# Performance work log

Measured on AMD Instinct MI355X. Metric: run time of the kernel, lower is better.

The kernel has to match this reference:

```python
import jax, jax.numpy as jnp
import numpy as np
import math

B, Q, CQ = 2, 2048, 512
H, D = 8, 64  # no_heads, c_hidden

def setup_inputs() -> dict:
    key = jax.random.key(0)
    ks = jax.random.split(key, 8)
    s = 0.02
    return {
        "q_x": jax.random.normal(ks[0], (B, Q, CQ), jnp.float32),
        "kv_x": jax.random.normal(ks[1], (B, Q, CQ), jnp.float32),
        "bias": jax.random.normal(ks[2], (B, 1, Q, Q), jnp.float32),
        "w_qkv": jax.random.normal(ks[3], (3 * H * D, CQ), jnp.float32) * s,
        "w_o": jax.random.normal(ks[4], (CQ, H * D), jnp.float32) * s,
        "b_o": jnp.zeros((CQ,), jnp.float32),
        "w_g": jax.random.normal(ks[5], (H * D, CQ), jnp.float32) * s,
        "b_g": jnp.zeros((H * D,), jnp.float32),
    }

def reference(q_x, kv_x, bias, w_qkv, w_o, b_o, w_g, b_g):
    # Fused QKV projection from q_x (kv_x is unused by the original module's _prep_qkv)
    qkv = jnp.einsum('bqc,ec->bqe', q_x, w_qkv)  # [B,Q,3*H*D]
    q, k, v = jnp.split(qkv, 3, axis=-1)
    q = q.reshape(B, Q, H, D) / math.sqrt(D)
    k = k.reshape(B, Q, H, D)
    v = v.reshape(B, Q, H, D)
    # scores + additive pairwise bias, softmax over keys
    scores = jnp.einsum('bqhd,bkhd->bhqk', q, k) + bias  # [B,H,Q,K]
    attn = jax.nn.softmax(scores, axis=-1)
    o = jnp.einsum('bhqk,bkhd->bqhd', attn, v)  # [B,Q,H,D]
    # sigmoid gating
    g = jax.nn.sigmoid(jnp.einsum('bqc,ec->bqe', q_x, w_g) + b_g).reshape(B, Q, H, D)
    o = o * g
    # output projection
    o = o.reshape(B, Q, H * D)
    return jnp.einsum('bqe,ce->bqc', o, w_o) + b_o
```

## Files before the change

### kernel.cpp

```cpp
#include <hip/hip_runtime.h>
#include <math.h>

#define B_  2
#define Q_  2048
#define CQ_ 512
#define H_  8
#define D_  64
#define M_  (B_*Q_)
#define L2E 1.44269504088896f

typedef __bf16 bf16;
typedef __bf16 bf16x4 __attribute__((ext_vector_type(4)));
typedef __bf16 bf16x8 __attribute__((ext_vector_type(8)));
typedef float  f32x4  __attribute__((ext_vector_type(4)));
typedef float  f32x16 __attribute__((ext_vector_type(16)));
typedef unsigned int u32x2 __attribute__((ext_vector_type(2)));

__device__ __forceinline__ void gl_lds16(const bf16* g, bf16* l) {
    __builtin_amdgcn_global_load_lds(
        (const __attribute__((address_space(1))) unsigned int*)g,
        (__attribute__((address_space(3))) unsigned int*)l, 16, 0, 0);
}

__device__ __forceinline__ unsigned int cvtpk_bf16(float lo, float hi) {
    unsigned int r;
    asm("v_cvt_pk_bf16_f32 %0, %1, %2" : "=v"(r) : "v"(lo), "v"(hi));
    return r;
}

#define S0 (4096*512)
#define S1 (1536*512)
#define S2 (512*512)
#define S3 (512*512)
#define NCV ((S0 + S1 + S2 + S3) / (256 * 8))
__global__ __launch_bounds__(256)
void convert_kernel(const float* __restrict__ qx, const float* __restrict__ wqkv,
                    const float* __restrict__ wg, const float* __restrict__ wo,
                    const float* __restrict__ bias,
                    bf16* __restrict__ qxb, bf16* __restrict__ wcat,
                    bf16* __restrict__ wob, float* __restrict__ bT)
{
    __shared__ float lds[2048];
    const int bx = blockIdx.x;
    const int t  = threadIdx.x;
    if (bx < NCV) {
        const long long e = ((long long)bx * 256 + t) * 8;
        const float* src; bf16* dst;
        if (e < S0)                { src = qx + e;                  dst = qxb + e; }
        else if (e < S0 + S1)      { src = wqkv + (e - S0);         dst = wcat + (e - S0); }
        else if (e < S0 + S1 + S2) { src = wg + (e - S0 - S1);      dst = wcat + S1 + (e - S0 - S1); }
        else                       { src = wo + (e - S0 - S1 - S2); dst = wob + (e - S0 - S1 - S2); }
        const float4 a = *(const float4*)(src);
        const float4 b = *(const float4*)(src + 4);
        bf16x8 v;
        v[0] = (bf16)a.x; v[1] = (bf16)a.y; v[2] = (bf16)a.z; v[3] = (bf16)a.w;
        v[4] = (bf16)b.x; v[5] = (bf16)b.y; v[6] = (bf16)b.z; v[7] = (bf16)b.w;
        *(bf16x8*)dst = v;
    } else {
        const int x = bx - NCV;
        const int b = x >> 11, q32 = (x >> 5) & 63, kt = x & 31;
        const int qo = t >> 3, kc = (t & 7) * 8;
        const float* src = bias + ((size_t)b * Q_ + q32 * 32 + qo) * Q_ + kt * 64 + kc;
        const float4 a = *(const float4*)src;
        const float4 c = *(const float4*)(src + 4);
        const float v[8] = {a.x, a.y, a.z, a.w, c.x, c.y, c.z, c.w};
        #pragma unroll
        for (int j2 = 0; j2 < 8; ++j2) {
            const int ko = kc + j2;
            const int i  = (ko >> 5) * 4 + ((ko >> 3) & 3);
            const int b5 = (ko >> 2) & 1;
            const int j  = ko & 3;
            lds[i * 256 + b5 * 128 + qo * 4 + j] = v[j2] * L2E;
        }
        __syncthreads();
        float* outp = bT + ((size_t)(b * 64 + q32) * 32 + kt) * 2048 + t * 8;
        *(float4*)(outp)     = *(const float4*)(lds + t * 8);
        *(float4*)(outp + 4) = *(const float4*)(lds + t * 8 + 4);
    }
}

template<int BM, int BN>
__global__ __launch_bounds__(256)
void gemm_bf16(const bf16* __restrict__ A, const bf16* __restrict__ W,
               const float* __restrict__ bvec,
               bf16* __restrict__ qb, bf16* __restrict__ kb, bf16* __restrict__ vb,
               bf16* __restrict__ gb)
{
    constexpr int MI = BM / 32, NJ = BN / 32;
    __shared__ __align__(16) bf16 As[BM * 32];
    __shared__ __align__(16) bf16 Bs[BN * 32];

    const int t = threadIdx.x;
    const int w = t >> 6, lane = t & 63;
    const int l15 = lane & 15, quad = lane >> 4;
    const int wm = w & 1, wn = w >> 1;
    const int bm = blockIdx.x * BM;
    const int bn = blockIdx.y * BN;
    const bool swapped = ((bn >> 9) != 2);

    f32x4 acc[MI][NJ] = {};

    const int rr = t >> 2;
    const int cc = (t & 3) * 8;

    for (int k0 = 0; k0 < 512; k0 += 32) {
        #pragma unroll
        for (int i = 0; i < BM / 64; ++i)
            gl_lds16(A + (size_t)(bm + i * 64 + rr) * 512 + k0 + cc,
                     As + (i * 64 + w * 16) * 32);
        #pragma unroll
        for (int i = 0; i < BN / 64; ++i)
            gl_lds16(W + (size_t)(bn + i * 64 + rr) * 512 + k0 + cc,
                     Bs + (i * 64 + w * 16) * 32);
        __asm__ volatile("s_waitcnt vmcnt(0)" ::: "memory");
        __syncthreads();

        bf16x8 af[MI], bfr[NJ];
        #pragma unroll
        for (int i = 0; i < MI; ++i)
            af[i] = *(const bf16x8*)(As + (wm * (BM / 2) + i * 16 + l15) * 32 + quad * 8);
        #pragma unroll
        for (int j = 0; j < NJ; ++j)
            bfr[j] = *(const bf16x8*)(Bs + (wn * (BN / 2) + j * 16 + l15) * 32 + quad * 8);
        if (swapped) {
            #pragma unroll
            for (int i = 0; i < MI; ++i)
                #pragma unroll
                for (int j = 0; j < NJ; ++j)
                    acc[i][j] = __builtin_amdgcn_mfma_f32_16x16x32_bf16(bfr[j], af[i], acc[i][j], 0, 0, 0);
        } else {
            #pragma unroll
            for (int i = 0; i < MI; ++i)
                #pragma unroll
                for (int j = 0; j < NJ; ++j)
                    acc[i][j] = __builtin_amdgcn_mfma_f32_16x16x32_bf16(af[i], bfr[j], acc[i][j], 0, 0, 0);
        }
        __syncthreads();
    }

    if (swapped) {
        #pragma unroll
        for (int i = 0; i < MI; ++i) {
            const int m = bm + wm * (BM / 2) + i * 16 + l15;
            const int b = m >> 11, qq = m & 2047;
            #pragma unroll
            for (int j = 0; j < NJ; ++j) {
                const int n0 = bn + wn * (BN / 2) + j * 16 + quad * 4;
                const f32x4 cv = acc[i][j];
                const int part = n0 >> 9;
                if (part == 0) {
                    const int h = (n0 >> 6) & 7, d0 = n0 & 63;
                    bf16x4 q4;
                    #pragma unroll
                    for (int r = 0; r < 4; ++r) q4[r] = (bf16)(cv[r] * (0.125f * L2E));
                    *(bf16x4*)(qb + (size_t)(b * H_ + h) * (Q_ * D_) + (size_t)qq * 64 + d0) = q4;
                } else if (part == 1) {
                    const int h = (n0 >> 6) & 7, d0 = n0 & 63;
                    const size_t off = (size_t)(b * H_ + h) * (Q_ * D_)
                        + (qq >> 6) * 4096 + ((qq >> 5) & 1) * 2048
                        + (d0 >> 4) * 512 + ((d0 >> 3) & 1) * 256
                        + (qq & 31) * 8 + (d0 & 7);
                    bf16x4 k4;
                    #pragma unroll
                    for (int r = 0; r < 4; ++r) k4[r] = (bf16)cv[r];
                    *(bf16x4*)(kb + off) = k4;
                } else {
                    const int gcol = n0 & 511;
                    const float4 bv4 = *(const float4*)(bvec + gcol);
                    bf16x4 g4;
                    g4[0] = (bf16)(1.f / (1.f + __expf(-(cv[0] + bv4.x))));
                    g4[1] = (bf16)(1.f / (1.f + __expf(-(cv[1] + bv4.y))));
                    g4[2] = (bf16)(1.f / (1.f + __expf(-(cv[2] + bv4.z))));
                    g4[3] = (bf16)(1.f / (1.f + __expf(-(cv[3] + bv4.w))));
                    *(bf16x4*)(gb + (size_t)m * 512 + gcol) = g4;
                }
            }
        }
    } else {
        #pragma unroll
        for (int i = 0; i < MI; ++i) {
            const int m0 = bm + wm * (BM / 2) + i * 16 + quad * 4;
            const int b = m0 >> 11, qq0 = m0 & 2047;
            #pragma unroll
            for (int j = 0; j < NJ; ++j) {
                const int n = bn + wn * (BN / 2) + j * 16 + l15;
                const int h = (n >> 6) & 7, d = n & 63;
                const size_t off = (size_t)(b * H_ + h) * (Q_ * D_)
                    + (qq0 >> 6) * 4096 + (d >> 5) * 2048
                    + ((qq0 & 63) >> 4) * 512 + ((qq0 >> 3) & 1) * 256
                    + (d & 31) * 8 + (qq0 & 7);
                bf16x4 v4;
                #pragma unroll
                for (int r = 0; r < 4; ++r) v4[r] = (bf16)acc[i][j][r];
                *(bf16x4*)(vb + off) = v4;
            }
        }
    }
}

__global__ __launch_bounds__(256, 3)
void attn_part(const bf16* __restrict__ qb, const bf16* __restrict__ kf,
               const bf16* __restrict__ vf, const float* __restrict__ bT,
               bf16* __restrict__ po, float2* __restrict__ ml)
{
    __shared__ __align__(16) bf16 Ks[2][4096];
    __shared__ __align__(16) bf16 Vs[2][4096];

    const int tid  = threadIdx.x;
    const int wv   = tid >> 6, lane = tid & 63;
    const int l31  = lane & 31, b5 = lane >> 5;
    const int x    = blockIdx.x;
    const int bh   = ((x & 7) << 1) | (x >> 3);
    const int b    = bh >> 3;
    const int qg   = blockIdx.y * 128 + wv * 32 + l31;
    const int ks   = blockIdx.z;
    const int t0   = ks * 11;
    const int nt   = (ks < 2) ? 11 : 10;

    const bf16* qp = qb + ((size_t)bh * Q_ + qg) * D_;
    bf16x8 bq[4];
    #pragma unroll
    for (int c = 0; c < 4; ++c)
        bq[c] = *(const bf16x8*)(qp + c * 16 + b5 * 8);

    f32x16 acc[2] = {};
    float m_run = -INFINITY, l_run = 0.f;

    const bf16*  kfb  = kf + (size_t)bh * (Q_ * D_) + (size_t)t0 * 4096;
    const bf16*  vfb  = vf + (size_t)bh * (Q_ * D_) + (size_t)t0 * 4096;
    const int q32 = blockIdx.y * 4 + wv;
    const float* brow = bT + (((size_t)b * 64 + q32) * 32 + t0) * 2048;

    f32x4 nb[8];

    #pragma unroll
    for (int p = 0; p < 2; ++p) {
        gl_lds16(kfb + (wv * 2 + p) * 512 + lane * 8, Ks[0] + (wv * 2 + p) * 512);
        gl_lds16(vfb + (wv * 2 + p) * 512 + lane * 8, Vs[0] + (wv * 2 + p) * 512);
    }
    #pragma unroll
    for (int i = 0; i < 8; ++i)
        nb[i] = *(const f32x4*)(brow + i * 256 + lane * 4);
    __asm__ volatile("s_waitcnt vmcnt(0)" ::: "memory");
    __syncthreads();

    int cur = 0;
    #pragma unroll 1
    for (int t = 0; t < nt; ++t) {
        if (t < nt - 1) {
            const size_t off = (size_t)(t + 1) * 4096;
            #pragma unroll
            for (int p = 0; p < 2; ++p) {
                gl_lds16(kfb + off + (wv * 2 + p) * 512 + lane * 8,
                         Ks[cur ^ 1] + (wv * 2 + p) * 512);
                gl_lds16(vfb + off + (wv * 2 + p) * 512 + lane * 8,
                         Vs[cur ^ 1] + (wv * 2 + p) * 512);
            }
        }
        __asm__ volatile("" ::: "memory");

        f32x16 sv[2];
        #pragma unroll
        for (int kg = 0; kg < 2; ++kg)
            #pragma unroll
            for (int r = 0; r < 16; ++r)
                sv[kg][r] = nb[kg * 4 + (r >> 2)][r & 3];

        if (t < nt - 1) {
            const float* bnx = brow + (size_t)(t + 1) * 2048;
            #pragma unroll
            for (int i = 0; i < 8; ++i)
                nb[i] = *(const f32x4*)(bnx + i * 256 + lane * 4);
        }
        __asm__ volatile("" ::: "memory");

        const bf16* Kc = Ks[cur];
        __builtin_amdgcn_s_setprio(1);
        #pragma unroll
        for (int kg = 0; kg < 2; ++kg)
            #pragma unroll
            for (int c = 0; c < 4; ++c) {
                const bf16x8 ak = *(const bf16x8*)(Kc + kg * 2048 + c * 512 + lane * 8);
                sv[kg] = __builtin_amdgcn_mfma_f32_32x32x16_bf16(ak, bq[c], sv[kg], 0, 0, 0);
            }
        __builtin_amdgcn_s_setprio(0);

        float mx[16];
        #pragma unroll
        for (int r = 0; r < 16; ++r) mx[r] = fmaxf(sv[0][r], sv[1][r]);
        #pragma unroll
        for (int r = 0; r < 8; ++r) mx[r] = fmaxf(mx[r], mx[r + 8]);
        #pragma unroll
        for (int r = 0; r < 4; ++r) mx[r] = fmaxf(mx[r], mx[r + 4]);
        float tmax = fmaxf(fmaxf(mx[0], mx[1]), fmaxf(mx[2], mx[3]));
        tmax = fmaxf(tmax, __shfl_xor(tmax, 32, 64));

        const float m_old = m_run;
        const bool keep = (__all(tmax <= m_old + 8.f) != 0);
        const float mn = keep ? m_old : fmaxf(m_old, tmax);
        m_run = mn;

        #pragma unroll
        for (int kg = 0; kg < 2; ++kg)
            #pragma unroll
            for (int r = 0; r < 16; ++r)
                sv[kg][r] = __builtin_amdgcn_exp2f(sv[kg][r] - mn);

        float sm[16];
        #pragma unroll
        for (int r = 0; r < 16; ++r) sm[r] = sv[0][r] + sv[1][r];
        #pragma unroll
        for (int r = 0; r < 8; ++r) sm[r] += sm[r + 8];
        #pragma unroll
        for (int r = 0; r < 4; ++r) sm[r] += sm[r + 4];
        float rsum = (sm[0] + sm[1]) + (sm[2] + sm[3]);
        rsum += __shfl_xor(rsum, 32, 64);
        if (keep) {
            l_run += rsum;
        } else {
            const float alpha = __builtin_amdgcn_exp2f(m_old - mn);
            l_run = l_run * alpha + rsum;
            acc[0] *= alpha;
            acc[1] *= alpha;
        }

        bf16x8 bp[4];
        #pragma unroll
        for (int kg = 0; kg < 2; ++kg)
            #pragma unroll
            for (int h = 0; h < 2; ++h) {
                const unsigned int u  = cvtpk_bf16(sv[kg][8 * h + 0], sv[kg][8 * h + 1]);
                const unsigned int u2 = cvtpk_bf16(sv[kg][8 * h + 2], sv[kg][8 * h + 3]);
                const unsigned int vv = cvtpk_bf16(sv[kg][8 * h + 4], sv[kg][8 * h + 5]);
                const unsigned int v2 = cvtpk_bf16(sv[kg][8 * h + 6], sv[kg][8 * h + 7]);
                const u32x2 s1 = __builtin_amdgcn_permlane32_swap(u,  vv, false, false);
                const u32x2 s2 = __builtin_amdgcn_permlane32_swap(u2, v2, false, false);
                union { unsigned int w[4]; bf16x8 v8; } pkw;
                pkw.w[0] = s1[0]; pkw.w[1] = s2[0]; pkw.w[2] = s1[1]; pkw.w[3] = s2[1];
                bp[kg * 2 + h] = pkw.v8;
            }

        const bf16* Vc = Vs[cur];
        __builtin_amdgcn_s_setprio(1);
        #pragma unroll
        for (int c4 = 0; c4 < 4; ++c4) {
            #pragma unroll
            for (int dg = 0; dg < 2; ++dg) {
                const bf16x8 av = *(const bf16x8*)(Vc + dg * 2048 + c4 * 512 + lane * 8);
                acc[dg] = __builtin_amdgcn_mfma_f32_32x32x16_bf16(av, bp[c4], acc[dg], 0, 0, 0);
            }
        }
        __builtin_amdgcn_s_setprio(0);

        __asm__ volatile("s_waitcnt vmcnt(8)" ::: "memory");
        __syncthreads();
        cur ^= 1;
    }

    const float inv = 1.f / l_run;
    const size_t pbase = ((size_t)(ks * 16 + bh) * Q_ + qg) * 64;
    #pragma unroll
    for (int dg = 0; dg < 2; ++dg)
        #pragma unroll
        for (int gi = 0; gi < 4; ++gi) {
            const int d0 = dg * 32 + gi * 8 + b5 * 4;
            bf16x4 ov;
            #pragma unroll
            for (int r = 0; r < 4; ++r)
                ov[r] = (bf16)(acc[dg][gi * 4 + r] * inv);
            *(bf16x4*)(po + pbase + d0) = ov;
        }
    if (b5 == 0)
        ml[(size_t)(ks * 16 + bh) * Q_ + qg] = make_float2(m_run, l_run);
}

__global__ __launch_bounds__(256)
void gemm_out(const bf16* __restrict__ po, const float2* __restrict__ ml,
              const bf16* __restrict__ gb, const bf16* __restrict__ W,
              const float* __restrict__ bvec, float* __restrict__ fout)
{
    constexpr int BM = 64, BN = 128, MI = BM / 32, NJ = BN / 32;
    __shared__ __align__(16) bf16 As[BM * 32];
    __shared__ __align__(16) bf16 Bs[BN * 32];

    const int t = threadIdx.x;
    const int w = t >> 6, lane = t & 63;
    const int l15 = lane & 15, quad = lane >> 4;
    const int wm = w & 1, wn = w >> 1;
    const int bm = blockIdx.x * BM;
    const int bn = blockIdx.y * BN;

    const int rr = t >> 2;
    const int cc = (t & 3) * 8;
    const int m  = bm + rr;
    const int b  = m >> 11, qq = m & 2047;

    f32x4 acc[MI][NJ] = {};

    for (int k0 = 0; k0 < 512; k0 += 32) {
        #pragma unroll
        for (int i = 0; i < BN / 64; ++i)
            gl_lds16(W + (size_t)(bn + i * 64 + rr) * 512 + k0 + cc,
                     Bs + (i * 64 + w * 16) * 32);

        {
            const int c0 = k0 + cc;
            const int h  = c0 >> 6, d8 = c0 & 63;
            const int prow = (b * 8 + h) * 2048 + qq;
            const float2 m0 = ml[prow];
            const float2 m1 = ml[32768 + prow];
            const float2 m2 = ml[65536 + prow];
            const float Mx = fmaxf(fmaxf(m0.x, m1.x), m2.x);
            float w0 = m0.y * __builtin_amdgcn_exp2f(m0.x - Mx);
            float w1 = m1.y * __builtin_amdgcn_exp2f(m1.x - Mx);
            float w2 = m2.y * __builtin_amdgcn_exp2f(m2.x - Mx);
            const float inv = 1.f / (w0 + w1 + w2);
            w0 *= inv; w1 *= inv; w2 *= inv;
            const bf16x8 p0 = *(const bf16x8*)(po + (size_t)prow * 64 + d8);
            const bf16x8 p1 = *(const bf16x8*)(po + (size_t)(32768 + prow) * 64 + d8);
            const bf16x8 p2 = *(const bf16x8*)(po + (size_t)(65536 + prow) * 64 + d8);
            const bf16x8 gv = *(const bf16x8*)(gb + (size_t)m * 512 + c0);
            bf16x8 av;
            #pragma unroll
            for (int r = 0; r < 8; ++r)
                av[r] = (bf16)(((float)p0[r] * w0 + (float)p1[r] * w1 +
                                (float)p2[r] * w2) * (float)gv[r]);
            *(bf16x8*)(As + t * 8) = av;
        }

        __asm__ volatile("s_waitcnt vmcnt(0)" ::: "memory");
        __syncthreads();

        bf16x8 af[MI], bfr[NJ];
        #pragma unroll
        for (int i = 0; i < MI; ++i)
            af[i] = *(const bf16x8*)(As + (wm * (BM / 2) + i * 16 + l15) * 32 + quad * 8);
        #pragma unroll
        for (int j = 0; j < NJ; ++j)
            bfr[j] = *(const bf16x8*)(Bs + (wn * (BN / 2) + j * 16 + l15) * 32 + quad * 8);
        #pragma unroll
        for (int i = 0; i < MI; ++i)
            #pragma unroll
            for (int j = 0; j < NJ; ++j)
                acc[i][j] = __builtin_amdgcn_mfma_f32_16x16x32_bf16(bfr[j], af[i], acc[i][j], 0, 0, 0);
        __syncthreads();
    }

    #pragma unroll
    for (int i = 0; i < MI; ++i) {
        const int mm = bm + wm * (BM / 2) + i * 16 + l15;
        #pragma unroll
        for (int j = 0; j < NJ; ++j) {
            const int n0 = bn + wn * (BN / 2) + j * 16 + quad * 4;
            const f32x4 cv = acc[i][j];
            float4 st;
            st.x = cv[0] + bvec[n0 + 0];
            st.y = cv[1] + bvec[n0 + 1];
            st.z = cv[2] + bvec[n0 + 2];
            st.w = cv[3] + bvec[n0 + 3];
            *(float4*)(fout + (size_t)mm * 512 + n0) = st;
        }
    }
}

extern "C" void kernel_launch(void* const* d_in, const int* in_sizes, int n_in,
                              void* d_out, int out_size, void* d_ws, size_t ws_size,
                              hipStream_t stream)
{
    const float* q_x   = (const float*)d_in[0];
    const float* bias  = (const float*)d_in[2];
    const float* w_qkv = (const float*)d_in[3];
    const float* w_o   = (const float*)d_in[4];
    const float* b_o   = (const float*)d_in[5];
    const float* w_g   = (const float*)d_in[6];
    const float* b_g   = (const float*)d_in[7];
    float* out = (float*)d_out;

    char* ws = (char*)d_ws;
    bf16*   qxb  = (bf16*)(ws);
    bf16*   wcat = (bf16*)(ws + (4u  << 20));
    bf16*   po   = (bf16*)(ws);
    bf16*   qb   = (bf16*)(ws + (16u << 20));
    bf16*   kb   = (bf16*)(ws + (20u << 20));
    bf16*   vb   = (bf16*)(ws + (24u << 20));
    bf16*   gb   = (bf16*)(ws + (28u << 20));
    bf16*   wob  = (bf16*)(ws + (36u << 20));
    float2* ml   = (float2*)(ws + (36u << 20) + (1u << 19));
    float*  bT   = (float*)(ws + (38u << 20));

    convert_kernel<<<NCV + B_ * 64 * 32, 256, 0, stream>>>(
        q_x, w_qkv, w_g, w_o, bias, qxb, wcat, wob, bT);
    gemm_bf16<128, 128><<<dim3(32, 16), 256, 0, stream>>>(
        qxb, wcat, b_g, qb, kb, vb, gb);
    attn_part<<<dim3(B_ * H_, Q_ / 128, 3), 256, 0, stream>>>(qb, kb, vb, bT, po, ml);
    gemm_out<<<dim3(64, 4), 256, 0, stream>>>(po, ml, gb, wob, b_o, out);
}
```

Before: 178.4 us.

## Ping-pong bias prefetch registers in attention, software-prefetch gated A operands in output GEMM

The attention loop is unrolled by two and alternates between two bias register sets, so the next tile's bias prefetch no longer needs a register copy. The row-max reduction is regrouped into three-input max chains, and the block barrier becomes explicit waitcnt plus s_barrier with scheduling fences. In the output projection GEMM, the partial outputs, softmax stats and gate loads for the next K-step are issued before the barrier. A partial vmcnt wait lets those loads overlap the MFMA work instead of stalling on vmcnt(0) every iteration. This raises register pressure, and the final prefetch reads slightly past the last iteration's data, possibly past the end of the gate buffer for the last row.

```diff
diff --git a/kernel.cpp b/kernel.cpp
--- a/kernel.cpp
+++ b/kernel.cpp
@@ -231,7 +231,7 @@
     const int q32 = blockIdx.y * 4 + wv;
     const float* brow = bT + (((size_t)b * 64 + q32) * 32 + t0) * 2048;
 
-    f32x4 nb[8];
+    f32x4 nbA[8], nbB[8];
 
     #pragma unroll
     for (int p = 0; p < 2; ++p) {
@@ -240,13 +240,12 @@
     }
     #pragma unroll
     for (int i = 0; i < 8; ++i)
-        nb[i] = *(const f32x4*)(brow + i * 256 + lane * 4);
+        nbA[i] = *(const f32x4*)(brow + i * 256 + lane * 4);
     __asm__ volatile("s_waitcnt vmcnt(0)" ::: "memory");
     __syncthreads();
 
-    int cur = 0;
-    #pragma unroll 1
-    for (int t = 0; t < nt; ++t) {
+    auto step = [&](int t, f32x4 (&nbc)[8], f32x4 (&nbn)[8]) {
+        const int cur = t & 1;
         if (t < nt - 1) {
             const size_t off = (size_t)(t + 1) * 4096;
             #pragma unroll
@@ -264,13 +263,13 @@
         for (int kg = 0; kg < 2; ++kg)
             #pragma unroll
             for (int r = 0; r < 16; ++r)
-                sv[kg][r] = nb[kg * 4 + (r >> 2)][r & 3];
+                sv[kg][r] = nbc[kg * 4 + (r >> 2)][r & 3];
 
         if (t < nt - 1) {
             const float* bnx = brow + (size_t)(t + 1) * 2048;
             #pragma unroll
             for (int i = 0; i < 8; ++i)
-                nb[i] = *(const f32x4*)(bnx + i * 256 + lane * 4);
+                nbn[i] = *(const f32x4*)(bnx + i * 256 + lane * 4);
         }
         __asm__ volatile("" ::: "memory");
 
@@ -285,14 +284,17 @@
             }
         __builtin_amdgcn_s_setprio(0);
 
-        float mx[16];
-        #pragma unroll
-        for (int r = 0; r < 16; ++r) mx[r] = fmaxf(sv[0][r], sv[1][r]);
-        #pragma unroll
-        for (int r = 0; r < 8; ++r) mx[r] = fmaxf(mx[r], mx[r + 8]);
-        #pragma unroll
-        for (int r = 0; r < 4; ++r) mx[r] = fmaxf(mx[r], mx[r + 4]);
-        float tmax = fmaxf(fmaxf(mx[0], mx[1]), fmaxf(mx[2], mx[3]));
+        float a[8];
+        #pragma unroll
+        for (int r = 0; r < 8; ++r)
+            a[r] = fmaxf(fmaxf(sv[0][r], sv[0][r + 8]), sv[1][r]);
+        #pragma unroll
+        for (int r = 0; r < 4; ++r)
+            a[r] = fmaxf(fmaxf(a[r], a[r + 4]), sv[1][8 + r]);
+        #pragma unroll
+        for (int r = 0; r < 4; ++r)
+            a[r] = fmaxf(a[r], sv[1][12 + r]);
+        float tmax = fmaxf(fmaxf(a[0], a[1]), fmaxf(a[2], a[3]));
         tmax = fmaxf(tmax, __shfl_xor(tmax, 32, 64));
 
         const float m_old = m_run;
@@ -352,10 +354,20 @@
         }
         __builtin_amdgcn_s_setprio(0);
 
-        __asm__ volatile("s_waitcnt vmcnt(8)" ::: "memory");
-        __syncthreads();
-        cur ^= 1;
-    }
+        __asm__ volatile("s_waitcnt vmcnt(8) lgkmcnt(0)" ::: "memory");
+        __builtin_amdgcn_sched_barrier(0);
+        __builtin_amdgcn_s_barrier();
+        __builtin_amdgcn_sched_barrier(0);
+    };
+
+    int t = 0;
+    #pragma unroll 1
+    for (; t + 1 < nt; t += 2) {
+        step(t,     nbA, nbB);
+        step(t + 1, nbB, nbA);
+    }
+    if (t < nt)
+        step(t, nbA, nbB);
 
     const float inv = 1.f / l_run;
     const size_t pbase = ((size_t)(ks * 16 + bh) * Q_ + qg) * 64;
@@ -397,6 +409,23 @@
 
     f32x4 acc[MI][NJ] = {};
 
+    float2 m0_, m1_, m2_;
+    bf16x8 p0_, p1_, p2_, gv_;
+    auto issueA = [&](int k0) {
+        const int c0 = k0 + cc;
+        const int h  = c0 >> 6, d8 = c0 & 63;
+        const int prow = (b * 8 + h) * 2048 + qq;
+        m0_ = ml[prow];
+        m1_ = ml[32768 + prow];
+        m2_ = ml[65536 + prow];
+        p0_ = *(const bf16x8*)(po + (size_t)prow * 64 + d8);
+        p1_ = *(const bf16x8*)(po + (size_t)(32768 + prow) * 64 + d8);
+        p2_ = *(const bf16x8*)(po + (size_t)(65536 + prow) * 64 + d8);
+        gv_ = *(const bf16x8*)(gb + (size_t)m * 512 + c0);
+    };
+
+    issueA(0);
+
     for (int k0 = 0; k0 < 512; k0 += 32) {
         #pragma unroll
         for (int i = 0; i < BN / 64; ++i)
@@ -404,32 +433,27 @@
                      Bs + (i * 64 + w * 16) * 32);
 
         {
-            const int c0 = k0 + cc;
-            const int h  = c0 >> 6, d8 = c0 & 63;
-            const int prow = (b * 8 + h) * 2048 + qq;
-            const float2 m0 = ml[prow];
-            const float2 m1 = ml[32768 + prow];
-            const float2 m2 = ml[65536 + prow];
-            const float Mx = fmaxf(fmaxf(m0.x, m1.x), m2.x);
-            float w0 = m0.y * __builtin_amdgcn_exp2f(m0.x - Mx);
-            float w1 = m1.y * __builtin_amdgcn_exp2f(m1.x - Mx);
-            float w2 = m2.y * __builtin_amdgcn_exp2f(m2.x - Mx);
+            const float Mx = fmaxf(fmaxf(m0_.x, m1_.x), m2_.x);
+            float w0 = m0_.y * __builtin_amdgcn_exp2f(m0_.x - Mx);
+            float w1 = m1_.y * __builtin_amdgcn_exp2f(m1_.x - Mx);
+            float w2 = m2_.y * __builtin_amdgcn_exp2f(m2_.x - Mx);
             const float inv = 1.f / (w0 + w1 + w2);
             w0 *= inv; w1 *= inv; w2 *= inv;
-            const bf16x8 p0 = *(const bf16x8*)(po + (size_t)prow * 64 + d8);
-            const bf16x8 p1 = *(const bf16x8*)(po + (size_t)(32768 + prow) * 64 + d8);
-            const bf16x8 p2 = *(const bf16x8*)(po + (size_t)(65536 + prow) * 64 + d8);
-            const bf16x8 gv = *(const bf16x8*)(gb + (size_t)m * 512 + c0);
             bf16x8 av;
             #pragma unroll
             for (int r = 0; r < 8; ++r)
-                av[r] = (bf16)(((float)p0[r] * w0 + (float)p1[r] * w1 +
-                                (float)p2[r] * w2) * (float)gv[r]);
+                av[r] = (bf16)(((float)p0_[r] * w0 + (float)p1_[r] * w1 +
+                                (float)p2_[r] * w2) * (float)gv_[r]);
             *(bf16x8*)(As + t * 8) = av;
         }
-
-        __asm__ volatile("s_waitcnt vmcnt(0)" ::: "memory");
-        __syncthreads();
+        __asm__ volatile("" ::: "memory");
+        issueA(k0 + 32);
+        __asm__ volatile("" ::: "memory");
+
+        __asm__ volatile("s_waitcnt vmcnt(7) lgkmcnt(0)" ::: "memory");
+        __builtin_amdgcn_sched_barrier(0);
+        __builtin_amdgcn_s_barrier();
+        __builtin_amdgcn_sched_barrier(0);
 
         bf16x8 af[MI], bfr[NJ];
         #pragma unroll
@@ -443,7 +467,11 @@
             #pragma unroll
             for (int j = 0; j < NJ; ++j)
                 acc[i][j] = __builtin_amdgcn_mfma_f32_16x16x32_bf16(bfr[j], af[i], acc[i][j], 0, 0, 0);
-        __syncthreads();
+
+        __asm__ volatile("s_waitcnt lgkmcnt(0)" ::: "memory");
+        __builtin_amdgcn_sched_barrier(0);
+        __builtin_amdgcn_s_barrier();
+        __builtin_amdgcn_sched_barrier(0);
     }
 
     #pragma unroll
```

After: 192.7 us. +8.0%, slower.
